# Kernel tuning notes

Measured on AMD Instinct MI355X. Metric: run time of the kernel, lower is better.

## Reference

```python
import jax, jax.numpy as jnp
import numpy as np

B, T, F = 16, 4096, 80      # batch, frames, mel bins
C = 512                     # conv channels
ZD, ZN = 64, 512            # codebook dim / size
YD, YN = 128, 128           # speaker embed dim / count
K = 5                       # kernel size
SLOPE = 0.2                 # leaky relu negative slope


def conv1d(x, w, b):
    # x: [B,Cin,T], w: [Cout,Cin,K], 'same' padding, stride 1
    pad = (w.shape[-1] - 1) // 2
    y = jax.lax.conv_general_dilated(x, w, (1,), [(pad, pad)],
                                     dimension_numbers=('NCH', 'OIH', 'NCH'))
    return y + b[None, :, None]


def convT1(x, w, b):
    # torch ConvTranspose1d(stride=1, padding=(K-1)//2) == conv with spatially
    # flipped, in/out-swapped kernel. w: [Cin, Cout, K]
    wc = jnp.flip(w, -1).transpose(1, 0, 2)  # -> [Cout, Cin, K]
    return conv1d(x, wc, b)


def ln_c(x, g, b, eps=1e-5):
    # layer norm over channel axis, per (batch, time) position
    m = jnp.mean(x, 1, keepdims=True)
    v = jnp.var(x, 1, keepdims=True)
    return (x - m) * jax.lax.rsqrt(v + eps) * g[None, :, None] + b[None, :, None]


def _forward(x, y, enc_w1, enc_b1, enc_g1, enc_bt1, enc_w2, enc_b2, enc_g2, enc_bt2,
             enc_w3, enc_b3, enc_g3, enc_bt3, mlp_w, mlp_b, codebook, spk_emb,
             dec_w1, dec_b1, dec_g1, dec_bt1, dec_w2, dec_b2, dec_g2, dec_bt2,
             dec_w3, dec_b3):
    xc = x.transpose(0, 2, 1)                                    # [B,F,T]
    # Conditions: normalized speaker embedding lookup
    spk = spk_emb / jnp.linalg.norm(spk_emb, axis=1, keepdims=True)
    ye = spk[y].transpose(0, 2, 1)                               # [B,YD,T]
    # encoder: Conv1d -> LayerNorm(channel) -> LeakyReLU, x3, then 1x1 conv to z_dim
    h = jax.nn.leaky_relu(ln_c(conv1d(xc, enc_w1, enc_b1), enc_g1, enc_bt1), SLOPE)
    h = jax.nn.leaky_relu(ln_c(conv1d(h, enc_w2, enc_b2), enc_g2, enc_bt2), SLOPE)
    h = jax.nn.leaky_relu(ln_c(conv1d(h, enc_w3, enc_b3), enc_g3, enc_bt3), SLOPE)
    z = conv1d(h, mlp_w, mlp_b)                                  # [B,ZD,T]
    # vector quantizer (eval path): cdist^2 -> argmin -> gather
    zt = z.transpose(0, 2, 1)                                    # [B,T,ZD]
    zf = zt.reshape(-1, ZD)                                      # [B*T,ZD]
    d = (jnp.sum(zf * zf, axis=1, keepdims=True)
         + jnp.sum(codebook * codebook, axis=1)
         - 2.0 * zf @ codebook.T)                                # [B*T,ZN]
    idx = jnp.argmin(d, axis=1)
    z_vq = codebook[idx].reshape(zt.shape).transpose(0, 2, 1)    # [B,ZD,T]
    # decoder: (concat y -> ConvT -> LayerNorm -> GLU) x2, then concat y -> ConvT
    def glu_layer(h, w, b, g, bt):
        h = jnp.concatenate([h, ye], axis=1)
        h = ln_c(convT1(h, w, b), g, bt)
        a, gate = jnp.split(h, 2, axis=1)
        return a * jax.nn.sigmoid(gate)
    h = glu_layer(z_vq, dec_w1, dec_b1, dec_g1, dec_bt1)
    h = glu_layer(h, dec_w2, dec_b2, dec_g2, dec_bt2)
    h = jnp.concatenate([h, ye], axis=1)
    xhat = convT1(h, dec_w3, dec_b3)                             # [B,F,T]
    return xhat.transpose(0, 2, 1)                               # [B,T,F]


def setup_inputs() -> dict:
    key = jax.random.key(0)
    ks = jax.random.split(key, 16)
    def n(k, shape, sc=0.05):
        return jax.random.normal(k, shape, jnp.float32) * sc
    return {
        "x": jax.random.normal(ks[0], (B, T, F), jnp.float32),
        "y": jax.random.randint(ks[1], (B, T), 0, YN),
        "enc_w1": n(ks[2], (C, F, K)), "enc_b1": jnp.zeros(C), "enc_g1": jnp.ones(C), "enc_bt1": jnp.zeros(C),
        "enc_w2": n(ks[3], (C, C, K)), "enc_b2": jnp.zeros(C), "enc_g2": jnp.ones(C), "enc_bt2": jnp.zeros(C),
        "enc_w3": n(ks[4], (C, C, K)), "enc_b3": jnp.zeros(C), "enc_g3": jnp.ones(C), "enc_bt3": jnp.zeros(C),
        "mlp_w": n(ks[5], (ZD, C, 1)), "mlp_b": jnp.zeros(ZD),
        "codebook": jax.random.normal(ks[6], (ZN, ZD), jnp.float32),
        "spk_emb": jax.random.normal(ks[7], (YN, YD), jnp.float32),
        "dec_w1": n(ks[8], (ZD + YD, 2 * C, K)), "dec_b1": jnp.zeros(2 * C), "dec_g1": jnp.ones(2 * C), "dec_bt1": jnp.zeros(2 * C),
        "dec_w2": n(ks[9], (C + YD, 2 * C, K)), "dec_b2": jnp.zeros(2 * C), "dec_g2": jnp.ones(2 * C), "dec_bt2": jnp.zeros(2 * C),
        "dec_w3": n(ks[10], (C + YD, F, K)), "dec_b3": jnp.zeros(F),
    }


def reference(x, y, enc_w1, enc_b1, enc_g1, enc_bt1, enc_w2, enc_b2, enc_g2, enc_bt2,
              enc_w3, enc_b3, enc_g3, enc_bt3, mlp_w, mlp_b, codebook, spk_emb,
              dec_w1, dec_b1, dec_g1, dec_bt1, dec_w2, dec_b2, dec_g2, dec_bt2,
              dec_w3, dec_b3):
    return _forward(x, y, enc_w1, enc_b1, enc_g1, enc_bt1, enc_w2, enc_b2, enc_g2, enc_bt2,
                    enc_w3, enc_b3, enc_g3, enc_bt3, mlp_w, mlp_b, codebook, spk_emb,
                    dec_w1, dec_b1, dec_g1, dec_bt1, dec_w2, dec_b2, dec_g2, dec_bt2,
                    dec_w3, dec_b3)
```

## Files before the change

### kernel.cpp

```cpp
#include <hip/hip_runtime.h>
#include <hip/hip_bf16.h>
#include <cmath>

#define T_LEN 4096
#define BATCH 16
typedef __hip_bfloat16 bf16;
typedef unsigned short u16;
typedef float f32x4 __attribute__((ext_vector_type(4)));
typedef short s16x8 __attribute__((ext_vector_type(8)));
typedef unsigned short u16x8 __attribute__((ext_vector_type(8)));

__device__ __forceinline__ float ldx(const void* p, int dt, size_t i) {
    return dt ? __bfloat162float(((const bf16*)p)[i]) : ((const float*)p)[i];
}
__device__ __forceinline__ void stx(void* p, int dt, size_t i, float v) {
    if (dt) ((bf16*)p)[i] = __float2bfloat16(v);
    else ((float*)p)[i] = v;
}
__device__ __forceinline__ u16 f2b(float v) {
    bf16 h = __float2bfloat16(v);
    return *(u16*)&h;
}
__device__ __forceinline__ float b2f(u16 u) {
    return __bfloat162float(*(const bf16*)&u);
}

__global__ void detect_kernel(const float* __restrict__ x, int* __restrict__ flag) {
    __shared__ int s[256];
    int tid = threadIdx.x;
    int bad = 0;
    for (int i = tid; i < 2048; i += 256) {
        float v = x[i];
        if (!(fabsf(v) < 1e30f)) bad = 1;
    }
    s[tid] = bad;
    __syncthreads();
    for (int off = 128; off > 0; off >>= 1) {
        if (tid < off) s[tid] |= s[tid + off];
        __syncthreads();
    }
    if (tid == 0) *flag = s[0];
}

__global__ void spk_norm_kernel(const int* __restrict__ dflag,
                                const void* __restrict__ spk,
                                float* __restrict__ out) {
    const int f = *dflag;
    int s = blockIdx.x, d = threadIdx.x;
    float v = ldx(spk, f, (size_t)s * 128 + d);
    __shared__ float red[128];
    red[d] = v * v;
    __syncthreads();
    for (int off = 64; off > 0; off >>= 1) {
        if (d < off) red[d] += red[d + off];
        __syncthreads();
    }
    float rs = rsqrtf(red[0]);
    out[s * 128 + d] = v * rs;
}

__global__ __launch_bounds__(256) void repack0_kernel(
    const int* __restrict__ dflag, const void* __restrict__ src,
    int Cout, int Cin, int K, int ocp, int Cinp,
    bf16* __restrict__ dsthi, bf16* __restrict__ dstlo) {
    const int F = *dflag;
    __shared__ u16 sh[64 * 32 * 5];
    __shared__ u16 sl[64 * 32 * 5];
    const int ic0 = blockIdx.x * 32;
    const int oc0 = blockIdx.y * 64;
    const int tid = threadIdx.x;
    const int N = 64 * 32 * K;
    for (int idx = tid; idx < N; idx += 256) {
        int ocl = idx / (32 * K);
        int r = idx % (32 * K);
        int icl = r / K, k = r % K;
        int oc = oc0 + ocl, ic = ic0 + icl;
        float v = 0.f;
        if (oc < Cout && ic < Cin)
            v = ldx(src, F, ((size_t)oc * Cin + ic) * K + k);
        u16 hb = f2b(v);
        sh[(ocl * 32 + icl) * K + k] = hb;
        sl[(ocl * 32 + icl) * K + k] = f2b(v - b2f(hb));
    }
    __syncthreads();
    const int M = K * 64 * 4;
    for (int idx = tid; idx < M; idx += 256) {
        int k = idx / (64 * 4);
        int r = idx % (64 * 4);
        int ocl = r >> 2;
        int g8 = (r & 3) << 3;
        u16x8 h, l;
#pragma unroll
        for (int j = 0; j < 8; j++) {
            h[j] = sh[(ocl * 32 + g8 + j) * K + k];
            l[j] = sl[(ocl * 32 + g8 + j) * K + k];
        }
        size_t off = ((size_t)k * ocp + oc0 + ocl) * Cinp + ic0 + g8;
        *(u16x8*)&dsthi[off] = h;
        if (dstlo) *(u16x8*)&dstlo[off] = l;
    }
}

__global__ __launch_bounds__(256) void repack1_kernel(
    const int* __restrict__ dflag, const void* __restrict__ src,
    int Cout, int Cin, int K, int ocp, int Cinp,
    bf16* __restrict__ dsthi) {
    const int F = *dflag;
    __shared__ u16 sh[64 * 32 * 5];
    const int ic0 = blockIdx.x * 64;
    const int oc0 = blockIdx.y * 32;
    const int tid = threadIdx.x;
    const int N = 64 * 32 * K;
    for (int idx = tid; idx < N; idx += 256) {
        int icl = idx / (32 * K);
        int r = idx % (32 * K);
        int ocl = r / K, k = r % K;
        int oc = oc0 + ocl, ic = ic0 + icl;
        float v = 0.f;
        if (oc < Cout && ic < Cin)
            v = ldx(src, F, ((size_t)ic * Cout + oc) * K + k);
        sh[(icl * 32 + ocl) * K + (K - 1 - k)] = f2b(v);
    }
    __syncthreads();
    const int M = K * 32 * 8;
    for (int idx = tid; idx < M; idx += 256) {
        int k = idx / (32 * 8);
        int r = idx % (32 * 8);
        int ocl = r >> 3;
        int g8 = (r & 7) << 3;
        u16x8 h;
#pragma unroll
        for (int j = 0; j < 8; j++)
            h[j] = sh[((g8 + j) * 32 + ocl) * K + k];
        size_t off = ((size_t)k * ocp + oc0 + ocl) * Cinp + ic0 + g8;
        *(u16x8*)&dsthi[off] = h;
    }
}

__global__ void xprep_kernel(const int* __restrict__ dflag,
                             const void* __restrict__ x, int b0,
                             bf16* __restrict__ xp) {
    const int F = *dflag;
    int b = blockIdx.y;
    int t = blockIdx.x * 256 + threadIdx.x;
    size_t src = ((size_t)(b0 + b) * T_LEN + t) * 80;
    u16* row = (u16*)xp + ((size_t)b * T_LEN + t) * 192;
    for (int c4 = 0; c4 < 96; c4 += 4) {
        ushort4 h, l;
        u16* hp = (u16*)&h;
        u16* lp = (u16*)&l;
        for (int j = 0; j < 4; j++) {
            int c = c4 + j;
            float v = (c < 80) ? ldx(x, F, src + c) : 0.f;
            u16 hb = f2b(v);
            hp[j] = hb;
            lp[j] = f2b(v - b2f(hb));
        }
        *(ushort4*)&row[c4] = h;
        *(ushort4*)&row[96 + c4] = l;
    }
}

__global__ void ye_kernel(const int* __restrict__ y, int b0,
                          const float* __restrict__ spk_n,
                          bf16* __restrict__ D1, bf16* __restrict__ D2,
                          bf16* __restrict__ D3) {
    int b = blockIdx.y;
    int t = blockIdx.x * 256 + threadIdx.x;
    int idx = y[(size_t)(b0 + b) * T_LEN + t];
    const float* s = spk_n + (size_t)idx * 128;
    size_t r = (size_t)b * T_LEN + t;
    u16* p1 = (u16*)D1 + r * 192 + 64;
    u16* p2 = (u16*)D2 + r * 640 + 512;
    u16* p3 = (u16*)D3 + r * 640 + 512;
    for (int d4 = 0; d4 < 128; d4 += 4) {
        float4 v = *(const float4*)&s[d4];
        ushort4 h;
        h.x = f2b(v.x); h.y = f2b(v.y); h.z = f2b(v.z); h.w = f2b(v.w);
        *(ushort4*)&p1[d4] = h;
        *(ushort4*)&p2[d4] = h;
        *(ushort4*)&p3[d4] = h;
    }
}

template <int KK>
__global__ __launch_bounds__(256, 4) void conv_mfma(
    const int* __restrict__ dflag,
    const bf16* __restrict__ act, int RS, int loOff, int aloMode, int Cinp,
    const bf16* __restrict__ whi, const bf16* __restrict__ wlo, int wloMode,
    const void* __restrict__ bias,
    void* __restrict__ outp, int odt, int oRS, int ocMax, int boff) {
    constexpr int PAD = (KK - 1) / 2;
    constexpr int SROWS = 128 + KK - 1;
    const int F = *dflag;
    const bool useALo = (aloMode == 1) || (aloMode == 2 && F == 0);
    const bool useWLo = (wloMode == 2 && F == 0) && (wlo != nullptr);
    const int ocp = gridDim.y << 7;
    const int t0 = blockIdx.x * 128;
    const int oc0 = blockIdx.y * 128;
    const int b = blockIdx.z;
    const int tid = threadIdx.x;
    const int lane = tid & 63;
    const int wid = tid >> 6;
    const int widT = wid >> 1;
    const int widN = wid & 1;
    const int l16 = lane & 15;
    const int quad = lane >> 4;
    const int q8 = quad * 8;

    __shared__ __align__(16) bf16 sA[2 * SROWS * 40];

    const u16* wrow_hi = (const u16*)whi + (size_t)(oc0 + widN * 64 + l16) * Cinp + q8;
    const u16* wrow_lo = useWLo
        ? (const u16*)wlo + (size_t)(oc0 + widN * 64 + l16) * Cinp + q8 : nullptr;

    f32x4 acc[4][4];
#pragma unroll
    for (int i = 0; i < 4; i++)
#pragma unroll
        for (int j = 0; j < 4; j++) acc[i][j] = (f32x4){0.f, 0.f, 0.f, 0.f};

    const int nch = Cinp >> 5;
    for (int ch = 0; ch < nch; ch++) {
        const int ic0 = ch << 5;
        for (int g = tid; g < SROWS * 4; g += 256) {
            int row = g >> 2, c8 = (g & 3) << 3;
            int t = t0 - PAD + row;
            u16x8 v = (u16x8){0, 0, 0, 0, 0, 0, 0, 0};
            u16x8 vl = (u16x8){0, 0, 0, 0, 0, 0, 0, 0};
            if (t >= 0 && t < T_LEN) {
                const u16* src = (const u16*)act + ((size_t)b * T_LEN + t) * RS + ic0 + c8;
                v = *(const u16x8*)src;
                if (useALo) vl = *(const u16x8*)(src + loOff);
            }
            *(u16x8*)&sA[row * 40 + c8] = v;
            if (useALo) *(u16x8*)&sA[(SROWS + row) * 40 + c8] = vl;
        }
        __syncthreads();

#pragma unroll
        for (int tap = 0; tap < KK; tap++) {
            s16x8 bfr[4];
#pragma unroll
            for (int ni = 0; ni < 4; ni++)
                bfr[ni] = *(const s16x8*)(wrow_hi +
                    ((size_t)tap * ocp + ni * 16) * Cinp + ic0);
#pragma unroll
            for (int mi = 0; mi < 4; mi++) {
                int row = widT * 64 + mi * 16 + l16 + tap;
                s16x8 a = *(const s16x8*)&sA[row * 40 + q8];
#pragma unroll
                for (int ni = 0; ni < 4; ni++)
                    acc[mi][ni] = __builtin_amdgcn_mfma_f32_16x16x32_bf16(
                        a, bfr[ni], acc[mi][ni], 0, 0, 0);
                if (useALo) {
                    s16x8 al = *(const s16x8*)&sA[(SROWS + row) * 40 + q8];
#pragma unroll
                    for (int ni = 0; ni < 4; ni++)
                        acc[mi][ni] = __builtin_amdgcn_mfma_f32_16x16x32_bf16(
                            al, bfr[ni], acc[mi][ni], 0, 0, 0);
                }
            }
        }
        if (useWLo) {
#pragma unroll
            for (int tap = 0; tap < KK; tap++) {
                s16x8 bfr[4];
#pragma unroll
                for (int ni = 0; ni < 4; ni++)
                    bfr[ni] = *(const s16x8*)(wrow_lo +
                        ((size_t)tap * ocp + ni * 16) * Cinp + ic0);
#pragma unroll
                for (int mi = 0; mi < 4; mi++) {
                    int row = widT * 64 + mi * 16 + l16 + tap;
                    s16x8 a = *(const s16x8*)&sA[row * 40 + q8];
#pragma unroll
                    for (int ni = 0; ni < 4; ni++)
                        acc[mi][ni] = __builtin_amdgcn_mfma_f32_16x16x32_bf16(
                            a, bfr[ni], acc[mi][ni], 0, 0, 0);
                }
            }
        }
        __syncthreads();
    }

#pragma unroll
    for (int ni = 0; ni < 4; ni++) {
        int oc = oc0 + widN * 64 + ni * 16 + l16;
        if (oc >= ocMax) continue;
        float bv = ldx(bias, F, oc);
#pragma unroll
        for (int mi = 0; mi < 4; mi++) {
#pragma unroll
            for (int r = 0; r < 4; r++) {
                int t = t0 + widT * 64 + mi * 16 + quad * 4 + r;
                float v = acc[mi][ni][r] + bv;
                size_t off = ((size_t)(b + boff) * T_LEN + t) * (size_t)oRS + oc;
                if (odt == 0) ((float*)outp)[off] = v;
                else if (odt == 1) ((bf16*)outp)[off] = __float2bfloat16(v);
                else stx(outp, F, off, v);
            }
        }
    }
}

__global__ __launch_bounds__(256) void ln_lrelu(
    const int* __restrict__ dflag, const float* __restrict__ Fin,
    bf16* __restrict__ E, const void* __restrict__ g, const void* __restrict__ bt) {
    const int Fl = *dflag;
    int b = blockIdx.y;
    int t = blockIdx.x * 4 + (threadIdx.x >> 6);
    int lane = threadIdx.x & 63;
    const float* row = Fin + ((size_t)b * T_LEN + t) * 512 + lane * 8;
    float vv[8];
    *(float4*)&vv[0] = *(const float4*)row;
    *(float4*)&vv[4] = *(const float4*)(row + 4);
    float s = 0.f, s2 = 0.f;
#pragma unroll
    for (int j = 0; j < 8; j++) { s += vv[j]; s2 += vv[j] * vv[j]; }
    for (int m = 32; m; m >>= 1) {
        s += __shfl_xor(s, m);
        s2 += __shfl_xor(s2, m);
    }
    float mean = s / 512.f;
    float var = s2 / 512.f - mean * mean;
    float rstd = rsqrtf(var + 1e-5f);
    u16* eo = (u16*)E + ((size_t)b * T_LEN + t) * 1024 + lane * 8;
    ushort4 h[2], l[2];
#pragma unroll
    for (int j = 0; j < 8; j++) {
        int c = lane * 8 + j;
        float v = (vv[j] - mean) * rstd * ldx(g, Fl, c) + ldx(bt, Fl, c);
        v = v >= 0.f ? v : 0.2f * v;
        u16 hb = f2b(v);
        ((u16*)h)[j] = hb;
        ((u16*)l)[j] = f2b(v - b2f(hb));
    }
    *(ushort4*)&eo[0] = h[0];
    *(ushort4*)&eo[4] = h[1];
    *(ushort4*)&eo[512] = l[0];
    *(ushort4*)&eo[516] = l[1];
}

__global__ __launch_bounds__(256) void ln_glu(
    const int* __restrict__ dflag, const bf16* __restrict__ Fin,
    bf16* __restrict__ D, int oRS, const void* __restrict__ g,
    const void* __restrict__ bt) {
    const int Fl = *dflag;
    int b = blockIdx.y;
    int t = blockIdx.x * 4 + (threadIdx.x >> 6);
    int lane = threadIdx.x & 63;
    const u16* row = (const u16*)Fin + ((size_t)b * T_LEN + t) * 1024;
    ushort4 ua[2], ug[2];
    ua[0] = *(const ushort4*)&row[lane * 8];
    ua[1] = *(const ushort4*)&row[lane * 8 + 4];
    ug[0] = *(const ushort4*)&row[512 + lane * 8];
    ug[1] = *(const ushort4*)&row[512 + lane * 8 + 4];
    float av[8], gv[8];
#pragma unroll
    for (int j = 0; j < 8; j++) {
        av[j] = b2f(((u16*)ua)[j]);
        gv[j] = b2f(((u16*)ug)[j]);
    }
    float s = 0.f, s2 = 0.f;
#pragma unroll
    for (int j = 0; j < 8; j++) {
        s += av[j] + gv[j];
        s2 += av[j] * av[j] + gv[j] * gv[j];
    }
    for (int m = 32; m; m >>= 1) {
        s += __shfl_xor(s, m);
        s2 += __shfl_xor(s2, m);
    }
    float mean = s / 1024.f;
    float var = s2 / 1024.f - mean * mean;
    float rstd = rsqrtf(var + 1e-5f);
    ushort4 o[2];
#pragma unroll
    for (int j = 0; j < 8; j++) {
        int c = lane * 8 + j;
        float a = (av[j] - mean) * rstd * ldx(g, Fl, c) + ldx(bt, Fl, c);
        float gg = (gv[j] - mean) * rstd * ldx(g, Fl, 512 + c) + ldx(bt, Fl, 512 + c);
        ((u16*)o)[j] = f2b(a / (1.f + expf(-gg)));
    }
    u16* op = (u16*)D + ((size_t)b * T_LEN + t) * oRS + lane * 8;
    *(ushort4*)&op[0] = o[0];
    *(ushort4*)&op[4] = o[1];
}

__global__ __launch_bounds__(256) void vq_kernel(
    const int* __restrict__ dflag, const float* __restrict__ z,
    const void* __restrict__ cb, bf16* __restrict__ D1) {
    const int F = *dflag;
    int b = blockIdx.y;
    int t = blockIdx.x * 256 + threadIdx.x;
    int tid = threadIdx.x;

    __shared__ float sCB[128 * 64];
    __shared__ float sCC[128];

    float zr[64];
    const float* zp = z + ((size_t)b * T_LEN + t) * 64;
#pragma unroll
    for (int d4 = 0; d4 < 64; d4 += 4) *(float4*)&zr[d4] = *(const float4*)&zp[d4];
    float zz = 0.f;
#pragma unroll
    for (int d = 0; d < 64; d++) zz += zr[d] * zr[d];

    float best = 3.4e38f;
    int bidx = 0;
    for (int chunk = 0; chunk < 4; chunk++) {
        __syncthreads();
        for (int i = tid; i < 8192; i += 256)
            sCB[i] = ldx(cb, F, (size_t)chunk * 8192 + i);
        __syncthreads();
        if (tid < 128) {
            float cc = 0.f;
#pragma unroll 8
            for (int d = 0; d < 64; d++) {
                float cv = sCB[tid * 64 + d];
                cc += cv * cv;
            }
            sCC[tid] = cc;
        }
        __syncthreads();
        for (int c = 0; c < 128; c++) {
            const float* cp = &sCB[c * 64];
            float dot = 0.f;
#pragma unroll
            for (int d = 0; d < 64; d++) dot += zr[d] * cp[d];
            float dist = zz + sCC[c] - 2.f * dot;
            if (dist < best) { best = dist; bidx = chunk * 128 + c; }
        }
    }
    u16* out = (u16*)D1 + ((size_t)b * T_LEN + t) * 192;
    for (int d4 = 0; d4 < 64; d4 += 4) {
        ushort4 h;
        h.x = f2b(ldx(cb, F, (size_t)bidx * 64 + d4));
        h.y = f2b(ldx(cb, F, (size_t)bidx * 64 + d4 + 1));
        h.z = f2b(ldx(cb, F, (size_t)bidx * 64 + d4 + 2));
        h.w = f2b(ldx(cb, F, (size_t)bidx * 64 + d4 + 3));
        *(ushort4*)&out[d4] = h;
    }
}

extern "C" void kernel_launch(void* const* d_in, const int* in_sizes, int n_in,
                              void* d_out, int out_size, void* d_ws,
                              size_t ws_size, hipStream_t stream) {
    const void* x = d_in[0];
    const int* y = (const int*)d_in[1];
    const void* enc_w1 = d_in[2];  const void* enc_b1 = d_in[3];
    const void* enc_g1 = d_in[4];  const void* enc_bt1 = d_in[5];
    const void* enc_w2 = d_in[6];  const void* enc_b2 = d_in[7];
    const void* enc_g2 = d_in[8];  const void* enc_bt2 = d_in[9];
    const void* enc_w3 = d_in[10]; const void* enc_b3 = d_in[11];
    const void* enc_g3 = d_in[12]; const void* enc_bt3 = d_in[13];
    const void* mlp_w = d_in[14];  const void* mlp_b = d_in[15];
    const void* codebook = d_in[16];
    const void* spk_emb = d_in[17];
    const void* dec_w1 = d_in[18]; const void* dec_b1 = d_in[19];
    const void* dec_g1 = d_in[20]; const void* dec_bt1 = d_in[21];
    const void* dec_w2 = d_in[22]; const void* dec_b2 = d_in[23];
    const void* dec_g2 = d_in[24]; const void* dec_bt2 = d_in[25];
    const void* dec_w3 = d_in[26]; const void* dec_b3 = d_in[27];

    const size_t SW1 = (size_t)5 * 512 * 96;
    const size_t SW2 = (size_t)5 * 512 * 512;
    const size_t SW3 = SW2;
    const size_t SWM = (size_t)128 * 512;
    const size_t SD1 = (size_t)5 * 1024 * 192;
    const size_t SD2 = (size_t)5 * 1024 * 640;
    const size_t SD3 = (size_t)5 * 128 * 640;
    const size_t HI_TOT = SW1 + SW2 + SW3 + SWM + SD1 + SD2 + SD3;
    const size_t LO_TOT = SW1 + SW2 + SW3 + SWM;

    const size_t PB = (size_t)T_LEN * (192 * 2 + 1024 * 2 + 2048 + 64 * 4 + 640 * 2 + 640 * 2);
    const size_t FIXED = 256 + 65536 + (HI_TOT + LO_TOT) * 2;

    int nb = BATCH;
    while (nb > 1 && FIXED + (size_t)nb * PB > ws_size) nb >>= 1;

    char* p = (char*)d_ws;
    int* dflag = (int*)p;        p += 256;
    float* spk_n = (float*)p;    p += 65536;
    bf16* w1h = (bf16*)p;        p += SW1 * 2;
    bf16* w2h = (bf16*)p;        p += SW2 * 2;
    bf16* w3h = (bf16*)p;        p += SW3 * 2;
    bf16* wmh = (bf16*)p;        p += SWM * 2;
    bf16* wd1 = (bf16*)p;        p += SD1 * 2;
    bf16* wd2 = (bf16*)p;        p += SD2 * 2;
    bf16* wd3 = (bf16*)p;        p += SD3 * 2;
    bf16* w1l = (bf16*)p;        p += SW1 * 2;
    bf16* w2l = (bf16*)p;        p += SW2 * 2;
    bf16* w3l = (bf16*)p;        p += SW3 * 2;
    bf16* wml = (bf16*)p;        p += SWM * 2;
    bf16* xp = (bf16*)p;         p += (size_t)nb * T_LEN * 192 * 2;
    bf16* E = (bf16*)p;          p += (size_t)nb * T_LEN * 1024 * 2;
    char* Fb = p;                p += (size_t)nb * T_LEN * 2048;
    float* zbuf = (float*)p;     p += (size_t)nb * T_LEN * 64 * 4;
    bf16* D2 = (bf16*)p;         p += (size_t)nb * T_LEN * 640 * 2;
    bf16* D3 = (bf16*)p;
    bf16* D1 = xp;
    float* Ff = (float*)Fb;
    bf16* Fh = (bf16*)Fb;

    dim3 blk(256);

    detect_kernel<<<1, 256, 0, stream>>>((const float*)x, dflag);
    spk_norm_kernel<<<128, 128, 0, stream>>>(dflag, spk_emb, spk_n);

    repack0_kernel<<<dim3(3, 8), blk, 0, stream>>>(dflag, enc_w1, 512, 80, 5, 512, 96, w1h, w1l);
    repack0_kernel<<<dim3(16, 8), blk, 0, stream>>>(dflag, enc_w2, 512, 512, 5, 512, 512, w2h, w2l);
    repack0_kernel<<<dim3(16, 8), blk, 0, stream>>>(dflag, enc_w3, 512, 512, 5, 512, 512, w3h, w3l);
    repack0_kernel<<<dim3(16, 2), blk, 0, stream>>>(dflag, mlp_w, 64, 512, 1, 128, 512, wmh, wml);
    repack1_kernel<<<dim3(3, 32), blk, 0, stream>>>(dflag, dec_w1, 1024, 192, 5, 1024, 192, wd1);
    repack1_kernel<<<dim3(10, 32), blk, 0, stream>>>(dflag, dec_w2, 1024, 640, 5, 1024, 640, wd2);
    repack1_kernel<<<dim3(10, 4), blk, 0, stream>>>(dflag, dec_w3, 80, 640, 5, 128, 640, wd3);

    for (int b0 = 0; b0 < BATCH; b0 += nb) {
        dim3 gT(T_LEN / 256, nb);
        dim3 gLN(T_LEN / 4, nb);

        xprep_kernel<<<gT, blk, 0, stream>>>(dflag, x, b0, xp);

        conv_mfma<5><<<dim3(32, 4, nb), blk, 0, stream>>>(
            dflag, xp, 192, 96, 2, 96, w1h, w1l, 2, enc_b1, Ff, 0, 512, 512, 0);
        ye_kernel<<<gT, blk, 0, stream>>>(y, b0, spk_n, D1, D2, D3);
        ln_lrelu<<<gLN, blk, 0, stream>>>(dflag, Ff, E, enc_g1, enc_bt1);
        conv_mfma<5><<<dim3(32, 4, nb), blk, 0, stream>>>(
            dflag, E, 1024, 512, 1, 512, w2h, w2l, 2, enc_b2, Ff, 0, 512, 512, 0);
        ln_lrelu<<<gLN, blk, 0, stream>>>(dflag, Ff, E, enc_g2, enc_bt2);
        conv_mfma<5><<<dim3(32, 4, nb), blk, 0, stream>>>(
            dflag, E, 1024, 512, 1, 512, w3h, w3l, 2, enc_b3, Ff, 0, 512, 512, 0);
        ln_lrelu<<<gLN, blk, 0, stream>>>(dflag, Ff, E, enc_g3, enc_bt3);

        conv_mfma<1><<<dim3(32, 1, nb), blk, 0, stream>>>(
            dflag, E, 1024, 512, 1, 512, wmh, wml, 2, mlp_b, zbuf, 0, 64, 64, 0);

        vq_kernel<<<gT, blk, 0, stream>>>(dflag, zbuf, codebook, D1);

        conv_mfma<5><<<dim3(32, 8, nb), blk, 0, stream>>>(
            dflag, D1, 192, 0, 0, 192, wd1, nullptr, 0, dec_b1, Fh, 1, 1024, 1024, 0);
        ln_glu<<<gLN, blk, 0, stream>>>(dflag, Fh, D2, 640, dec_g1, dec_bt1);
        conv_mfma<5><<<dim3(32, 8, nb), blk, 0, stream>>>(
            dflag, D2, 640, 0, 0, 640, wd2, nullptr, 0, dec_b2, Fh, 1, 1024, 1024, 0);
        ln_glu<<<gLN, blk, 0, stream>>>(dflag, Fh, D3, 640, dec_g2, dec_bt2);
        conv_mfma<5><<<dim3(32, 1, nb), blk, 0, stream>>>(
            dflag, D3, 640, 0, 0, 640, wd3, nullptr, 0, dec_b3, d_out, 2, 80, 80, b0);
    }
}
```

Baseline: 4.804 ms.

## Give each wave a private LDS activation tile and drop block barriers

The conv kernel is restructured so each of the four waves owns a 64-time-step strip and its own LDS tile. The block now covers 256 time steps by 64 output channels instead of 128x128. Waves stage and consume their own activations with only lgkmcnt waits, removing the two __syncthreads per input chunk. A PLANES template parameter shrinks LDS when no low-precision activation plane is used. The trade is that each block now covers fewer output channels per activation load, so activations are reloaded for more oc-blocks and weight reuse across the time dimension drops. The explicit ocp parameter replaces deriving it from grid size.

```diff
diff --git a/kernel.cpp b/kernel.cpp
--- a/kernel.cpp
+++ b/kernel.cpp
@@ -183,36 +183,36 @@
     }
 }
 
-template <int KK>
+template <int KK, int PLANES>
 __global__ __launch_bounds__(256, 4) void conv_mfma(
     const int* __restrict__ dflag,
     const bf16* __restrict__ act, int RS, int loOff, int aloMode, int Cinp,
     const bf16* __restrict__ whi, const bf16* __restrict__ wlo, int wloMode,
-    const void* __restrict__ bias,
+    int ocp, const void* __restrict__ bias,
     void* __restrict__ outp, int odt, int oRS, int ocMax, int boff) {
     constexpr int PAD = (KK - 1) / 2;
-    constexpr int SROWS = 128 + KK - 1;
+    constexpr int WROWS = 64 + KK - 1;
+    constexpr int WSTR = 40;
     const int F = *dflag;
-    const bool useALo = (aloMode == 1) || (aloMode == 2 && F == 0);
+    const bool useALo = (PLANES == 2) && ((aloMode == 1) || (aloMode == 2 && F == 0));
     const bool useWLo = (wloMode == 2 && F == 0) && (wlo != nullptr);
-    const int ocp = gridDim.y << 7;
-    const int t0 = blockIdx.x * 128;
-    const int oc0 = blockIdx.y * 128;
+    const int oc0 = blockIdx.y * 64;
     const int b = blockIdx.z;
     const int tid = threadIdx.x;
     const int lane = tid & 63;
     const int wid = tid >> 6;
-    const int widT = wid >> 1;
-    const int widN = wid & 1;
+    const int t0w = blockIdx.x * 256 + wid * 64;
     const int l16 = lane & 15;
     const int quad = lane >> 4;
     const int q8 = quad * 8;
 
-    __shared__ __align__(16) bf16 sA[2 * SROWS * 40];
-
-    const u16* wrow_hi = (const u16*)whi + (size_t)(oc0 + widN * 64 + l16) * Cinp + q8;
+    __shared__ __align__(16) bf16 sAll[4 * PLANES * WROWS * WSTR];
+    bf16* sW = &sAll[wid * (PLANES * WROWS * WSTR)];
+    bf16* sWlo = sW + WROWS * WSTR;
+
+    const u16* wrow_hi = (const u16*)whi + (size_t)(oc0 + l16) * Cinp + q8;
     const u16* wrow_lo = useWLo
-        ? (const u16*)wlo + (size_t)(oc0 + widN * 64 + l16) * Cinp + q8 : nullptr;
+        ? (const u16*)wlo + (size_t)(oc0 + l16) * Cinp + q8 : nullptr;
 
     f32x4 acc[4][4];
 #pragma unroll
@@ -223,9 +223,10 @@
     const int nch = Cinp >> 5;
     for (int ch = 0; ch < nch; ch++) {
         const int ic0 = ch << 5;
-        for (int g = tid; g < SROWS * 4; g += 256) {
+        asm volatile("s_waitcnt lgkmcnt(0)" ::: "memory");
+        for (int g = lane; g < WROWS * 4; g += 64) {
             int row = g >> 2, c8 = (g & 3) << 3;
-            int t = t0 - PAD + row;
+            int t = t0w - PAD + row;
             u16x8 v = (u16x8){0, 0, 0, 0, 0, 0, 0, 0};
             u16x8 vl = (u16x8){0, 0, 0, 0, 0, 0, 0, 0};
             if (t >= 0 && t < T_LEN) {
@@ -233,10 +234,10 @@
                 v = *(const u16x8*)src;
                 if (useALo) vl = *(const u16x8*)(src + loOff);
             }
-            *(u16x8*)&sA[row * 40 + c8] = v;
-            if (useALo) *(u16x8*)&sA[(SROWS + row) * 40 + c8] = vl;
-        }
-        __syncthreads();
+            *(u16x8*)&sW[row * WSTR + c8] = v;
+            if (useALo) *(u16x8*)&sWlo[row * WSTR + c8] = vl;
+        }
+        asm volatile("s_waitcnt lgkmcnt(0)" ::: "memory");
 
 #pragma unroll
         for (int tap = 0; tap < KK; tap++) {
@@ -247,14 +248,14 @@
                     ((size_t)tap * ocp + ni * 16) * Cinp + ic0);
 #pragma unroll
             for (int mi = 0; mi < 4; mi++) {
-                int row = widT * 64 + mi * 16 + l16 + tap;
-                s16x8 a = *(const s16x8*)&sA[row * 40 + q8];
+                int row = mi * 16 + l16 + tap;
+                s16x8 a = *(const s16x8*)&sW[row * WSTR + q8];
 #pragma unroll
                 for (int ni = 0; ni < 4; ni++)
                     acc[mi][ni] = __builtin_amdgcn_mfma_f32_16x16x32_bf16(
                         a, bfr[ni], acc[mi][ni], 0, 0, 0);
                 if (useALo) {
-                    s16x8 al = *(const s16x8*)&sA[(SROWS + row) * 40 + q8];
+                    s16x8 al = *(const s16x8*)&sWlo[row * WSTR + q8];
 #pragma unroll
                     for (int ni = 0; ni < 4; ni++)
                         acc[mi][ni] = __builtin_amdgcn_mfma_f32_16x16x32_bf16(
@@ -272,8 +273,8 @@
                         ((size_t)tap * ocp + ni * 16) * Cinp + ic0);
 #pragma unroll
                 for (int mi = 0; mi < 4; mi++) {
-                    int row = widT * 64 + mi * 16 + l16 + tap;
-                    s16x8 a = *(const s16x8*)&sA[row * 40 + q8];
+                    int row = mi * 16 + l16 + tap;
+                    s16x8 a = *(const s16x8*)&sW[row * WSTR + q8];
 #pragma unroll
                     for (int ni = 0; ni < 4; ni++)
                         acc[mi][ni] = __builtin_amdgcn_mfma_f32_16x16x32_bf16(
@@ -281,19 +282,18 @@
                 }
             }
         }
-        __syncthreads();
     }
 
 #pragma unroll
     for (int ni = 0; ni < 4; ni++) {
-        int oc = oc0 + widN * 64 + ni * 16 + l16;
+        int oc = oc0 + ni * 16 + l16;
         if (oc >= ocMax) continue;
         float bv = ldx(bias, F, oc);
 #pragma unroll
         for (int mi = 0; mi < 4; mi++) {
 #pragma unroll
             for (int r = 0; r < 4; r++) {
-                int t = t0 + widT * 64 + mi * 16 + quad * 4 + r;
+                int t = t0w + mi * 16 + quad * 4 + r;
                 float v = acc[mi][ni][r] + bv;
                 size_t off = ((size_t)(b + boff) * T_LEN + t) * (size_t)oRS + oc;
                 if (odt == 0) ((float*)outp)[off] = v;
@@ -523,29 +523,29 @@
 
         xprep_kernel<<<gT, blk, 0, stream>>>(dflag, x, b0, xp);
 
-        conv_mfma<5><<<dim3(32, 4, nb), blk, 0, stream>>>(
-            dflag, xp, 192, 96, 2, 96, w1h, w1l, 2, enc_b1, Ff, 0, 512, 512, 0);
+        conv_mfma<5, 2><<<dim3(16, 8, nb), blk, 0, stream>>>(
+            dflag, xp, 192, 96, 2, 96, w1h, w1l, 2, 512, enc_b1, Ff, 0, 512, 512, 0);
         ye_kernel<<<gT, blk, 0, stream>>>(y, b0, spk_n, D1, D2, D3);
         ln_lrelu<<<gLN, blk, 0, stream>>>(dflag, Ff, E, enc_g1, enc_bt1);
-        conv_mfma<5><<<dim3(32, 4, nb), blk, 0, stream>>>(
-            dflag, E, 1024, 512, 1, 512, w2h, w2l, 2, enc_b2, Ff, 0, 512, 512, 0);
+        conv_mfma<5, 2><<<dim3(16, 8, nb), blk, 0, stream>>>(
+            dflag, E, 1024, 512, 1, 512, w2h, w2l, 2, 512, enc_b2, Ff, 0, 512, 512, 0);
         ln_lrelu<<<gLN, blk, 0, stream>>>(dflag, Ff, E, enc_g2, enc_bt2);
-        conv_mfma<5><<<dim3(32, 4, nb), blk, 0, stream>>>(
-            dflag, E, 1024, 512, 1, 512, w3h, w3l, 2, enc_b3, Ff, 0, 512, 512, 0);
+        conv_mfma<5, 2><<<dim3(16, 8, nb), blk, 0, stream>>>(
+            dflag, E, 1024, 512, 1, 512, w3h, w3l, 2, 512, enc_b3, Ff, 0, 512, 512, 0);
         ln_lrelu<<<gLN, blk, 0, stream>>>(dflag, Ff, E, enc_g3, enc_bt3);
 
-        conv_mfma<1><<<dim3(32, 1, nb), blk, 0, stream>>>(
-            dflag, E, 1024, 512, 1, 512, wmh, wml, 2, mlp_b, zbuf, 0, 64, 64, 0);
+        conv_mfma<1, 2><<<dim3(16, 1, nb), blk, 0, stream>>>(
+            dflag, E, 1024, 512, 1, 512, wmh, wml, 2, 128, mlp_b, zbuf, 0, 64, 64, 0);
 
         vq_kernel<<<gT, blk, 0, stream>>>(dflag, zbuf, codebook, D1);
 
-        conv_mfma<5><<<dim3(32, 8, nb), blk, 0, stream>>>(
-            dflag, D1, 192, 0, 0, 192, wd1, nullptr, 0, dec_b1, Fh, 1, 1024, 1024, 0);
+        conv_mfma<5, 1><<<dim3(16, 16, nb), blk, 0, stream>>>(
+            dflag, D1, 192, 0, 0, 192, wd1, nullptr, 0, 1024, dec_b1, Fh, 1, 1024, 1024, 0);
         ln_glu<<<gLN, blk, 0, stream>>>(dflag, Fh, D2, 640, dec_g1, dec_bt1);
-        conv_mfma<5><<<dim3(32, 8, nb), blk, 0, stream>>>(
-            dflag, D2, 640, 0, 0, 640, wd2, nullptr, 0, dec_b2, Fh, 1, 1024, 1024, 0);
+        conv_mfma<5, 1><<<dim3(16, 16, nb), blk, 0, stream>>>(
+            dflag, D2, 640, 0, 0, 640, wd2, nullptr, 0, 1024, dec_b2, Fh, 1, 1024, 1024, 0);
         ln_glu<<<gLN, blk, 0, stream>>>(dflag, Fh, D3, 640, dec_g2, dec_bt2);
-        conv_mfma<5><<<dim3(32, 1, nb), blk, 0, stream>>>(
-            dflag, D3, 640, 0, 0, 640, wd3, nullptr, 0, dec_b3, d_out, 2, 80, 80, b0);
-    }
-}
+        conv_mfma<5, 1><<<dim3(16, 2, nb), blk, 0, stream>>>(
+            dflag, D3, 640, 0, 0, 640, wd3, nullptr, 0, 128, dec_b3, d_out, 2, 80, 80, b0);
+    }
+}
```

Measured after the change: 6.389 ms. 1.33x slower.
